# Optimization experiments

Measured on AMD Instinct MI355X. Metric: run time of the kernel, lower is better.

## Reference

```python
import jax, jax.numpy as jnp
import numpy as np

B, N, IN_F, E, H, A = 8, 1024, 1024, 256, 4, 64
ALPHA = 0.2          # leaky relu slope
NEG = -9e15          # mask value from original code


def setup_inputs() -> dict:
    key = jax.random.key(0)
    k = jax.random.split(key, 7)
    x = jax.random.normal(k[0], (B * N, IN_F), dtype=jnp.float32)
    adj = jax.random.randint(k[1], (B, N, N), 0, 2, dtype=jnp.int32)
    # per-head GAT params: W (H, IN_F, E); a split into a1, a2 (H, E) each,
    # since cat([Wh_i, Wh_j]) @ a == Wh_i @ a1 + Wh_j @ a2 exactly.
    W = jax.random.normal(k[2], (H, IN_F, E), dtype=jnp.float32) * 0.05
    a1 = jax.random.normal(k[3], (H, E), dtype=jnp.float32) * 0.05
    a2 = jax.random.normal(k[4], (H, E), dtype=jnp.float32) * 0.05
    W_act = jax.random.normal(k[5], (H * E, A), dtype=jnp.float32) * 0.05
    b_act = jnp.zeros((A,), dtype=jnp.float32)
    return {"x": x, "adj": adj, "W": W, "a1": a1, "a2": a2,
            "W_act": W_act, "b_act": b_act}


def reference(x, adj, W, a1, a2, W_act, b_act):
    b, n, _ = adj.shape
    xr = x.reshape(b, n, -1)                                   # (B, N, IN_F)
    Wh = jnp.einsum('bni,hio->hbno', xr, W)                    # (H, B, N, E)
    f1 = jnp.einsum('hbno,ho->hbn', Wh, a1)                    # a . Wh_i part
    f2 = jnp.einsum('hbno,ho->hbn', Wh, a2)                    # a . Wh_j part
    e = jax.nn.leaky_relu(f1[..., :, None] + f2[..., None, :], ALPHA)  # (H,B,N,N)
    e = jnp.where(adj[None] > 0, e, NEG)
    att = jax.nn.softmax(e, axis=-1)                           # masked softmax
    h_prime = jnp.einsum('hbnm,hbmo->hbno', att, Wh)           # (H, B, N, E)
    h_prime = jax.nn.elu(h_prime)                              # concat=True -> elu
    feat = jnp.transpose(h_prime, (1, 2, 0, 3)).reshape(b * n, H * E)
    return feat @ W_act + b_act                                # (B*N, A)
```

## Files before the change

kernel.cpp:

```cpp
#include <hip/hip_runtime.h>
#include <stdint.h>

typedef __attribute__((ext_vector_type(8))) short short8;
typedef __attribute__((ext_vector_type(4))) float f32x4;
typedef __attribute__((ext_vector_type(16))) float f32x16;


__device__ __forceinline__ float b2f(unsigned short u) {
    union { unsigned int i; float f; } v; v.i = ((unsigned int)u) << 16; return v.f;
}
__device__ __forceinline__ unsigned short f2b(float f) {
    union { float f; unsigned int i; } v; v.f = f;
    unsigned int u = v.i;
    u = (u + 0x7FFFu + ((u >> 16) & 1u)) >> 16;
    return (unsigned short)u;
}
__device__ __forceinline__ void glds16(const void* g, const void* l) {
    __builtin_amdgcn_global_load_lds(
        (const __attribute__((address_space(1))) unsigned int*)g,
        (__attribute__((address_space(3))) unsigned int*)l, 16, 0, 0);
}

__device__ __forceinline__ void cvt8(const void* in, unsigned short* out,
                                     int f, int grp) {
    if (f) {
        ((ushort4*)out)[grp * 2]     = ((const ushort4*)in)[grp * 2];
        ((ushort4*)out)[grp * 2 + 1] = ((const ushort4*)in)[grp * 2 + 1];
    } else {
        const float4* p = (const float4*)in + (size_t)grp * 2;
        float4 a = p[0], b = p[1];
        ushort4 o0, o1;
        o0.x = f2b(a.x); o0.y = f2b(a.y); o0.z = f2b(a.z); o0.w = f2b(a.w);
        o1.x = f2b(b.x); o1.y = f2b(b.y); o1.z = f2b(b.z); o1.w = f2b(b.w);
        ((ushort4*)out)[grp * 2]     = o0;
        ((ushort4*)out)[grp * 2 + 1] = o1;
    }
}

__global__ void prep_small(const unsigned int* __restrict__ x,
                           const void* __restrict__ a1, const void* __restrict__ a2,
                           const void* __restrict__ bact,
                           unsigned short* __restrict__ a1b,
                           unsigned short* __restrict__ a2b,
                           unsigned short* __restrict__ bactb,
                           int* __restrict__ flag) {
    __shared__ int sflag;
    int tid = threadIdx.x;
    if (tid < 64) {
        unsigned int wv = x[tid];
        unsigned int e = (wv >> 7) & 0xFF;
        unsigned long long m = __ballot(e >= 100 && e <= 140);
        if (tid == 0) { sflag = (__popcll(m) >= 48) ? 1 : 0; flag[0] = sflag; }
    }
    __syncthreads();
    int f = sflag;
    if (tid < 128) cvt8(a1, a1b, f, tid);
    else           cvt8(a2, a2b, f, tid - 128);
    if (tid < 8)   cvt8(bact, bactb, f, tid);
}

__global__ void conv8(const void* __restrict__ in, unsigned short* __restrict__ out,
                      const int* __restrict__ flag, int total8) {
    int i = blockIdx.x * 256 + threadIdx.x;
    if (i >= total8) return;
    cvt8(in, out, *flag, i);
}

__global__ __launch_bounds__(256) void t2_all(
        const void* __restrict__ Win, const void* __restrict__ Wactin,
        unsigned short* __restrict__ WT, unsigned short* __restrict__ WactT,
        const int* __restrict__ flag) {
    __shared__ unsigned int tile[64 * 65];
    int z = blockIdx.z;
    const void* in; unsigned short* out; int C, bt;
    if (z < 4) { in = Win; out = WT; C = 256; bt = z; }
    else { if (blockIdx.x != 0) return; in = Wactin; out = WactT; C = 64; bt = 0; }
    int t = threadIdx.x;
    int c0 = blockIdx.x * 64;
    int r0 = blockIdx.y * 64;
    int rl = t >> 2;
    int cc = (t & 3) * 16;
    size_t ibase = ((size_t)bt * 1024 + (r0 + rl)) * C + c0 + cc;
    unsigned short v[16];
    if (*flag) {
        const unsigned short* p = (const unsigned short*)in + ibase;
        short8 a = *(const short8*)p;
        short8 b = *(const short8*)(p + 8);
#pragma unroll
        for (int j = 0; j < 8; j++) { v[j] = (unsigned short)a[j]; v[8 + j] = (unsigned short)b[j]; }
    } else {
        const float* p = (const float*)in + ibase;
#pragma unroll
        for (int j = 0; j < 16; j++) v[j] = f2b(p[j]);
    }
#pragma unroll
    for (int j = 0; j < 16; j++)
        tile[(cc + j) * 65 + rl] = v[j];
    __syncthreads();
    int cl = t >> 2;
    int rch = (t & 3) * 16;
    unsigned short o[16];
#pragma unroll
    for (int j = 0; j < 16; j++)
        o[j] = (unsigned short)tile[cl * 65 + rch + j];
    unsigned short* op = out + ((size_t)bt * C + (c0 + cl)) * 1024 + r0 + rch;
#pragma unroll
    for (int q = 0; q < 4; q++) {
        ushort4 s; s.x = o[q*4]; s.y = o[q*4+1]; s.z = o[q*4+2]; s.w = o[q*4+3];
        ((ushort4*)op)[q] = s;
    }
}

__global__ void pack_adj(const int* __restrict__ adj,
                         unsigned int* __restrict__ maskT) {
    int gid = blockIdx.x * 256 + threadIdx.x;
    int lane = threadIdx.x & 63;
    unsigned long long m = __ballot(adj[gid] > 0);
    if (lane == 0) {
        int lin = gid >> 6;
        int mw = (lin & 15) * 2;
        int bn = lin >> 4;
        int b = bn >> 10, n = bn & 1023;
        maskT[(size_t)(b * 32 + mw) * 1024 + n]     = (unsigned int)m;
        maskT[(size_t)(b * 32 + mw + 1) * 1024 + n] = (unsigned int)(m >> 32);
    }
}

__global__ __launch_bounds__(256) void k1_gemm(
        const unsigned short* __restrict__ x,
        const unsigned short* __restrict__ WT,
        unsigned short* __restrict__ WhF) {
    __shared__ unsigned short smA[8 * 512];
    __shared__ unsigned short smB[8 * 512];
    int tid = threadIdx.x;
    int w = tid >> 6, lane = tid & 63;
    int lr = lane & 15, lq = lane >> 4;
    int col0 = blockIdx.x * 128;
    int row0 = blockIdx.y * 128;
    int h = col0 >> 8;
    int e_base = col0 & 255;
    int b = row0 >> 10;
    int m_base = row0 & 1023;
    int wr = w >> 1, wc = w & 1;

    f32x4 acc[4][4] = {};

    for (int k0 = 0; k0 < 1024; k0 += 32) {
        __syncthreads();
#pragma unroll
        for (int s = 0; s < 2; s++) {
            int g = 2 * w + s;
            const unsigned short* srcA =
                x + (size_t)(row0 + g * 16 + lr) * 1024 + k0 + lq * 8;
            glds16(srcA, &smA[g * 512]);
            const unsigned short* srcB =
                WT + (size_t)(h * 256 + e_base + g * 16 + lr) * 1024 + k0 + lq * 8;
            glds16(srcB, &smB[g * 512]);
        }
        __syncthreads();
        short8 af[4], bf[4];
#pragma unroll
        for (int i = 0; i < 4; i++)
            af[i] = *(const short8*)&smA[(wr * 4 + i) * 512 + lane * 8];
#pragma unroll
        for (int j = 0; j < 4; j++)
            bf[j] = *(const short8*)&smB[(wc * 4 + j) * 512 + lane * 8];
#pragma unroll
        for (int i = 0; i < 4; i++)
#pragma unroll
            for (int j = 0; j < 4; j++)
                acc[i][j] = __builtin_amdgcn_mfma_f32_16x16x32_bf16(
                    af[i], bf[j], acc[i][j], 0, 0, 0);
    }

    int hb = h * 8 + b;
#pragma unroll
    for (int i = 0; i < 4; i++) {
#pragma unroll
        for (int j = 0; j < 4; j++) {
            int e = e_base + (wc * 4 + j) * 16 + lr;
            int et = e >> 5, e31 = e & 31;
            int m16 = (m_base >> 4) + wr * 4 + i;
            ushort4 vs;
            vs.x = f2b(acc[i][j][0]);
            vs.y = f2b(acc[i][j][1]);
            vs.z = f2b(acc[i][j][2]);
            vs.w = f2b(acc[i][j][3]);
            size_t idx = ((size_t)((hb * 8 + et) * 64 + m16) * 512)
                         + ((lq >> 1) * 32 + e31) * 8 + (lq & 1) * 4;
            *(ushort4*)&WhF[idx] = vs;
        }
    }
}

__global__ void k1b_f12(const unsigned short* __restrict__ WhF,
                        const unsigned short* __restrict__ a1,
                        const unsigned short* __restrict__ a2,
                        float* __restrict__ f1, float* __restrict__ f2) {
    int hb = blockIdx.y;
    int n = blockIdx.x * 256 + threadIdx.x;
    int h = hb >> 3;
    int m16 = n >> 4, l5m = (n >> 3) & 1, m7 = n & 7;
    const unsigned short* base = WhF + (size_t)hb * 8 * 64 * 512
                                 + (size_t)(l5m * 32) * 8 + m7;
    float s1 = 0.f, s2 = 0.f;
    for (int e = 0; e < 256; e++) {
        int et = e >> 5, e31 = e & 31;
        float wv = b2f(base[(size_t)(et * 64 + m16) * 512 + e31 * 8]);
        s1 += wv * b2f(a1[h * 256 + e]);
        s2 += wv * b2f(a2[h * 256 + e]);
    }
    f1[hb * 1024 + n] = s1;
    f2[hb * 1024 + n] = s2;
}

__global__ __launch_bounds__(256, 2) void k2_attn(
        const unsigned short* __restrict__ WhF,
        const unsigned int* __restrict__ maskT,
        const float* __restrict__ f1, const float* __restrict__ f2,
        unsigned short* __restrict__ feat) {
    int tid = threadIdx.x;
    int w = tid >> 6, lane = tid & 63;
    int l5 = lane >> 5, l31 = lane & 31;
    int bid = blockIdx.x;
    int xcd = bid & 7, idx = bid >> 3;
    int hb = xcd + 8 * (idx >> 4);
    int sub = idx & 15;
    int wid = sub * 4 + w;
    int rg = wid >> 1;
    int ehalf = wid & 1;
    int n0 = rg * 32;
    int h = hb >> 3, b = hb & 7;
    int row = n0 + l31;
    float f1n = f1[hb * 1024 + row];
    const unsigned short* whb = WhF + (size_t)(hb * 8 + ehalf * 4) * 64 * 512
                                + lane * 8;
    const unsigned int* mrow = maskT + (size_t)b * 32 * 1024 + row;
    const float* f2row = f2 + hb * 1024;

    f32x16 acc[4] = {};
    float den = 0.f;

    short8 buf[2][4][2];
#pragma unroll
    for (int et = 0; et < 4; et++)
#pragma unroll
        for (int ks = 0; ks < 2; ks++)
            buf[0][et][ks] = *(const short8*)(whb + (size_t)(et * 64 + ks) * 512);

#pragma unroll 2
    for (int m0 = 0; m0 < 1024; m0 += 32) {
        int p = (m0 >> 5) & 1;
        if (m0 + 32 < 1024) {
            int m16n = (m0 >> 4) + 2;
#pragma unroll
            for (int et = 0; et < 4; et++)
#pragma unroll
                for (int ks = 0; ks < 2; ks++)
                    buf[p ^ 1][et][ks] =
                        *(const short8*)(whb + (size_t)(et * 64 + m16n + ks) * 512);
        }
        unsigned int mw = mrow[(size_t)(m0 >> 5) * 1024];
        float4 fA0 = *(const float4*)(f2row + m0 + l5 * 8);
        float4 fA1 = *(const float4*)(f2row + m0 + l5 * 8 + 4);
        float4 fB0 = *(const float4*)(f2row + m0 + 16 + l5 * 8);
        float4 fB1 = *(const float4*)(f2row + m0 + 16 + l5 * 8 + 4);
        float fm[16] = {fA0.x,fA0.y,fA0.z,fA0.w, fA1.x,fA1.y,fA1.z,fA1.w,
                        fB0.x,fB0.y,fB0.z,fB0.w, fB1.x,fB1.y,fB1.z,fB1.w};
        short8 af[2];
#pragma unroll
        for (int ks = 0; ks < 2; ks++) {
#pragma unroll
            for (int j = 0; j < 8; j++) {
                float t_ = f1n + fm[ks * 8 + j];
                float e_ = fmaxf(t_, 0.2f * t_);
                float pv = ((mw >> (ks * 16 + l5 * 8 + j)) & 1u) ? __expf(e_) : 0.f;
                unsigned short pb = f2b(pv);
                af[ks][j] = (short)pb;
                den += b2f(pb);
            }
        }
#pragma unroll
        for (int et = 0; et < 4; et++)
#pragma unroll
            for (int ks = 0; ks < 2; ks++)
                acc[et] = __builtin_amdgcn_mfma_f32_32x32x16_bf16(
                    af[ks], buf[p][et][ks], acc[et], 0, 0, 0);
    }

    den += __shfl_xor(den, 32, 64);

#pragma unroll
    for (int reg = 0; reg < 16; reg++) {
        int r = (reg & 3) + 8 * (reg >> 2) + 4 * l5;
        float dr = __shfl(den, r, 64);
        float rdr = 1.0f / dr;
        int nn = n0 + r;
#pragma unroll
        for (int et = 0; et < 4; et++) {
            int e = ehalf * 128 + et * 32 + l31;
            float v = acc[et][reg] * rdr;
            float o = v > 0.f ? v : __expf(v) - 1.f;
            feat[(size_t)(b * 1024 + nn) * 1024 + h * 256 + e] = f2b(o);
        }
    }
}

__global__ __launch_bounds__(256) void k3_out(
        const unsigned short* __restrict__ feat,
        const unsigned short* __restrict__ WactT,
        const unsigned short* __restrict__ bact,
        void* __restrict__ out, const int* __restrict__ flag) {
    __shared__ unsigned short smA[2 * 512];
    __shared__ unsigned short smB[4 * 512];
    int tid = threadIdx.x;
    int w = tid >> 6, lane = tid & 63;
    int lr = lane & 15, lq = lane >> 4;
    int row0 = blockIdx.x * 32;
    int g = w & 1, ch = w >> 1;
    int bf16out = *flag;
    f32x4 acc[2] = {};

    for (int k0 = 0; k0 < 1024; k0 += 32) {
        __syncthreads();
        if (w < 2) {
            const unsigned short* src =
                feat + (size_t)(row0 + w * 16 + lr) * 1024 + k0 + lq * 8;
            glds16(src, &smA[w * 512]);
        } else {
#pragma unroll
            for (int s = 0; s < 2; s++) {
                int t = (w - 2) * 2 + s;
                const unsigned short* src =
                    WactT + (size_t)(t * 16 + lr) * 1024 + k0 + lq * 8;
                glds16(src, &smB[t * 512]);
            }
        }
        __syncthreads();
        short8 af = *(const short8*)&smA[g * 512 + lane * 8];
#pragma unroll
        for (int j = 0; j < 2; j++) {
            short8 bf = *(const short8*)&smB[(ch * 2 + j) * 512 + lane * 8];
            acc[j] = __builtin_amdgcn_mfma_f32_16x16x32_bf16(af, bf, acc[j], 0, 0, 0);
        }
    }
#pragma unroll
    for (int j = 0; j < 2; j++) {
        int col = ch * 32 + j * 16 + lr;
        float bv = b2f(bact[col]);
#pragma unroll
        for (int rr = 0; rr < 4; rr++) {
            int r = row0 + g * 16 + lq * 4 + rr;
            float val = acc[j][rr] + bv;
            if (bf16out) ((unsigned short*)out)[(size_t)r * 64 + col] = f2b(val);
            else         ((float*)out)[(size_t)r * 64 + col] = val;
        }
    }
}

extern "C" void kernel_launch(void* const* d_in, const int* in_sizes, int n_in,
                              void* d_out, int out_size, void* d_ws, size_t ws_size,
                              hipStream_t stream) {
    const void* x    = d_in[0];
    const int*  adj  = (const int*)d_in[1];
    const void* W    = d_in[2];
    const void* a1   = d_in[3];
    const void* a2   = d_in[4];
    const void* Wact = d_in[5];
    const void* bact = d_in[6];

    char* ws = (char*)d_ws;
    unsigned short* WhF   = (unsigned short*)(ws);
    unsigned short* xb    = (unsigned short*)(ws + 16777216);
    unsigned short* feat  = (unsigned short*)(ws + 16777216);
    unsigned short* WT    = (unsigned short*)(ws + 33554432);
    unsigned int*   maskT = (unsigned int*)(ws + 33554432);
    unsigned short* WactT = (unsigned short*)(ws + 35651584);
    float*          f1    = (float*)(ws + 35782656);
    float*          f2    = (float*)(ws + 35913728);
    unsigned short* a1b   = (unsigned short*)(ws + 36044800);
    unsigned short* a2b   = (unsigned short*)(ws + 36046848);
    unsigned short* bactb = (unsigned short*)(ws + 36048896);
    int*            flag  = (int*)(ws + 36049024);
    if (ws_size < (size_t)36049040) return;

    prep_small<<<1, 256, 0, stream>>>((const unsigned int*)x, a1, a2, bact,
                                      a1b, a2b, bactb, flag);
    conv8<<<4096, 256, 0, stream>>>(x, xb, flag, 1048576);
    t2_all<<<dim3(4, 16, 5), 256, 0, stream>>>(W, Wact, WT, WactT, flag);
    k1_gemm<<<dim3(8, 64), 256, 0, stream>>>(xb, WT, WhF);
    pack_adj<<<32768, 256, 0, stream>>>(adj, maskT);
    k1b_f12<<<dim3(4, 32), 256, 0, stream>>>(WhF, a1b, a2b, f1, f2);
    k2_attn<<<512, 256, 0, stream>>>(WhF, maskT, f1, f2, feat);
    k3_out<<<256, 256, 0, stream>>>(feat, WactT, bactb, d_out, flag);
}
```

Baseline: 239.8 us.

## Split attention key range across wave pairs and vectorise f1/f2 with atomics

The attention kernel changes from splitting the embedding dimension across waves to splitting the key range in halves. Each wave now computes all 256 output columns for half the keys, so the softmax weights are computed once per row instead of twice. Partial accumulators and denominators are combined through shared memory, which costs extra LDS traffic, higher register pressure from 8 accumulators, and the loss of the explicit double-buffered prefetch. The f1/f2 kernel now uses vectorised short8 loads split over embedding chunks and combines them with atomic adds, which needs a new zeroing kernel. It also pre-scales f1/f2 by log2(e) so exp2f can replace __expf, and the bf16 conversion becomes truncation instead of round-to-nearest.

```diff
diff --git a/kernel.cpp b/kernel.cpp
--- a/kernel.cpp
+++ b/kernel.cpp
@@ -64,6 +64,10 @@
     int i = blockIdx.x * 256 + threadIdx.x;
     if (i >= total8) return;
     cvt8(in, out, *flag, i);
+}
+
+__global__ void zero_kern(float4* __restrict__ p) {
+    p[blockIdx.x * 256 + threadIdx.x] = float4{0.f, 0.f, 0.f, 0.f};
 }
 
 __global__ __launch_bounds__(256) void t2_all(
@@ -198,20 +202,31 @@
                         const unsigned short* __restrict__ a2,
                         float* __restrict__ f1, float* __restrict__ f2) {
     int hb = blockIdx.y;
-    int n = blockIdx.x * 256 + threadIdx.x;
+    int ec = blockIdx.x;
+    int t = threadIdx.x;
     int h = hb >> 3;
-    int m16 = n >> 4, l5m = (n >> 3) & 1, m7 = n & 7;
     const unsigned short* base = WhF + (size_t)hb * 8 * 64 * 512
-                                 + (size_t)(l5m * 32) * 8 + m7;
-    float s1 = 0.f, s2 = 0.f;
-    for (int e = 0; e < 256; e++) {
+        + (size_t)(t >> 1) * 512 + ((t & 1) * 32) * 8;
+    float s1[8] = {}, s2[8] = {};
+    for (int ee = 0; ee < 64; ee++) {
+        int e = ec * 64 + ee;
         int et = e >> 5, e31 = e & 31;
-        float wv = b2f(base[(size_t)(et * 64 + m16) * 512 + e31 * 8]);
-        s1 += wv * b2f(a1[h * 256 + e]);
-        s2 += wv * b2f(a2[h * 256 + e]);
-    }
-    f1[hb * 1024 + n] = s1;
-    f2[hb * 1024 + n] = s2;
+        float a1e = b2f(a1[h * 256 + e]);
+        float a2e = b2f(a2[h * 256 + e]);
+        short8 v = *(const short8*)(base + (size_t)(et * 64) * 512 + e31 * 8);
+#pragma unroll
+        for (int j = 0; j < 8; j++) {
+            float wv = b2f((unsigned short)v[j]);
+            s1[j] += wv * a1e;
+            s2[j] += wv * a2e;
+        }
+    }
+    const float LOG2E = 1.44269504f;
+#pragma unroll
+    for (int j = 0; j < 8; j++) {
+        atomicAdd(&f1[hb * 1024 + t * 8 + j], s1[j] * LOG2E);
+        atomicAdd(&f2[hb * 1024 + t * 8 + j], s2[j] * LOG2E);
+    }
 }
 
 __global__ __launch_bounds__(256, 2) void k2_attn(
@@ -219,89 +234,102 @@
         const unsigned int* __restrict__ maskT,
         const float* __restrict__ f1, const float* __restrict__ f2,
         unsigned short* __restrict__ feat) {
+    __shared__ float cmb[4][64][65];
+    __shared__ float dend[4][32];
     int tid = threadIdx.x;
     int w = tid >> 6, lane = tid & 63;
     int l5 = lane >> 5, l31 = lane & 31;
     int bid = blockIdx.x;
     int xcd = bid & 7, idx = bid >> 3;
     int hb = xcd + 8 * (idx >> 4);
-    int sub = idx & 15;
-    int wid = sub * 4 + w;
-    int rg = wid >> 1;
-    int ehalf = wid & 1;
+    int pair = idx & 15;
+    int rg = pair * 2 + (w & 1);
+    int mh = w >> 1;
     int n0 = rg * 32;
     int h = hb >> 3, b = hb & 7;
     int row = n0 + l31;
     float f1n = f1[hb * 1024 + row];
-    const unsigned short* whb = WhF + (size_t)(hb * 8 + ehalf * 4) * 64 * 512
-                                + lane * 8;
+    const unsigned short* whb = WhF + (size_t)hb * 8 * 64 * 512 + lane * 8;
     const unsigned int* mrow = maskT + (size_t)b * 32 * 1024 + row;
     const float* f2row = f2 + hb * 1024;
 
-    f32x16 acc[4] = {};
+    f32x16 acc[8] = {};
     float den = 0.f;
 
-    short8 buf[2][4][2];
-#pragma unroll
-    for (int et = 0; et < 4; et++)
-#pragma unroll
-        for (int ks = 0; ks < 2; ks++)
-            buf[0][et][ks] = *(const short8*)(whb + (size_t)(et * 64 + ks) * 512);
-
-#pragma unroll 2
-    for (int m0 = 0; m0 < 1024; m0 += 32) {
-        int p = (m0 >> 5) & 1;
-        if (m0 + 32 < 1024) {
-            int m16n = (m0 >> 4) + 2;
-#pragma unroll
-            for (int et = 0; et < 4; et++)
-#pragma unroll
-                for (int ks = 0; ks < 2; ks++)
-                    buf[p ^ 1][et][ks] =
-                        *(const short8*)(whb + (size_t)(et * 64 + m16n + ks) * 512);
-        }
-        unsigned int mw = mrow[(size_t)(m0 >> 5) * 1024];
+    int m_lo = mh * 512, m_hi = m_lo + 512;
+    for (int m0 = m_lo; m0 < m_hi; m0 += 32) {
+        int m16 = m0 >> 4;
+        short8 fr[8][2];
+#pragma unroll
+        for (int et = 0; et < 8; et++)
+#pragma unroll
+            for (int ks = 0; ks < 2; ks++)
+                fr[et][ks] = *(const short8*)(whb + (size_t)(et * 64 + m16 + ks) * 512);
+
+        unsigned int mws = mrow[(size_t)(m0 >> 5) * 1024] >> (l5 * 8);
         float4 fA0 = *(const float4*)(f2row + m0 + l5 * 8);
         float4 fA1 = *(const float4*)(f2row + m0 + l5 * 8 + 4);
         float4 fB0 = *(const float4*)(f2row + m0 + 16 + l5 * 8);
         float4 fB1 = *(const float4*)(f2row + m0 + 16 + l5 * 8 + 4);
         float fm[16] = {fA0.x,fA0.y,fA0.z,fA0.w, fA1.x,fA1.y,fA1.z,fA1.w,
                         fB0.x,fB0.y,fB0.z,fB0.w, fB1.x,fB1.y,fB1.z,fB1.w};
-        short8 af[2];
+        union { unsigned int u[4]; short8 v; } af[2];
 #pragma unroll
         for (int ks = 0; ks < 2; ks++) {
 #pragma unroll
-            for (int j = 0; j < 8; j++) {
-                float t_ = f1n + fm[ks * 8 + j];
-                float e_ = fmaxf(t_, 0.2f * t_);
-                float pv = ((mw >> (ks * 16 + l5 * 8 + j)) & 1u) ? __expf(e_) : 0.f;
-                unsigned short pb = f2b(pv);
-                af[ks][j] = (short)pb;
-                den += b2f(pb);
+            for (int pr = 0; pr < 4; pr++) {
+                unsigned int ub[2];
+#pragma unroll
+                for (int q = 0; q < 2; q++) {
+                    int j = pr * 2 + q;
+                    float tL = f1n + fm[ks * 8 + j];
+                    float eL = fmaxf(tL, 0.2f * tL);
+                    float pv = ((mws >> (ks * 16 + j)) & 1u) ? exp2f(eL) : 0.f;
+                    union { float f; unsigned int i; } pu; pu.f = pv;
+                    ub[q] = pu.i & 0xFFFF0000u;
+                    union { unsigned int i; float f; } tb; tb.i = ub[q];
+                    den += tb.f;
+                }
+                af[ks].u[pr] = (ub[0] >> 16) | ub[1];
             }
         }
 #pragma unroll
-        for (int et = 0; et < 4; et++)
+        for (int et = 0; et < 8; et++)
 #pragma unroll
             for (int ks = 0; ks < 2; ks++)
                 acc[et] = __builtin_amdgcn_mfma_f32_32x32x16_bf16(
-                    af[ks], buf[p][et][ks], acc[et], 0, 0, 0);
+                    af[ks].v, fr[et][ks], acc[et], 0, 0, 0);
     }
 
     den += __shfl_xor(den, 32, 64);
 
+    int give = (mh == 0) ? 4 : 0;
+    int keep = (mh == 0) ? 0 : 4;
+#pragma unroll
+    for (int t = 0; t < 4; t++)
+#pragma unroll
+        for (int reg = 0; reg < 16; reg++)
+            cmb[w][lane][t * 16 + reg] = acc[give + t][reg];
+    if (lane < 32) dend[w][l31] = den;
+    __syncthreads();
+    int pw = w ^ 2;
+    float den_tot = den + dend[pw][l31];
+    float rdr_all[16];
 #pragma unroll
     for (int reg = 0; reg < 16; reg++) {
         int r = (reg & 3) + 8 * (reg >> 2) + 4 * l5;
-        float dr = __shfl(den, r, 64);
-        float rdr = 1.0f / dr;
-        int nn = n0 + r;
-#pragma unroll
-        for (int et = 0; et < 4; et++) {
-            int e = ehalf * 128 + et * 32 + l31;
-            float v = acc[et][reg] * rdr;
+        rdr_all[reg] = 1.0f / __shfl(den_tot, r, 64);
+    }
+#pragma unroll
+    for (int t = 0; t < 4; t++) {
+        int et = keep + t;
+        int e = et * 32 + l31;
+#pragma unroll
+        for (int reg = 0; reg < 16; reg++) {
+            int r = (reg & 3) + 8 * (reg >> 2) + 4 * l5;
+            float v = (acc[et][reg] + cmb[pw][lane][t * 16 + reg]) * rdr_all[reg];
             float o = v > 0.f ? v : __expf(v) - 1.f;
-            feat[(size_t)(b * 1024 + nn) * 1024 + h * 256 + e] = f2b(o);
+            feat[(size_t)(b * 1024 + n0 + r) * 1024 + h * 256 + e] = f2b(o);
         }
     }
 }
@@ -388,9 +416,10 @@
                                       a1b, a2b, bactb, flag);
     conv8<<<4096, 256, 0, stream>>>(x, xb, flag, 1048576);
     t2_all<<<dim3(4, 16, 5), 256, 0, stream>>>(W, Wact, WT, WactT, flag);
+    zero_kern<<<64, 256, 0, stream>>>((float4*)f1);
     k1_gemm<<<dim3(8, 64), 256, 0, stream>>>(xb, WT, WhF);
     pack_adj<<<32768, 256, 0, stream>>>(adj, maskT);
-    k1b_f12<<<dim3(4, 32), 256, 0, stream>>>(WhF, a1b, a2b, f1, f2);
+    k1b_f12<<<dim3(4, 32), 128, 0, stream>>>(WhF, a1b, a2b, f1, f2);
     k2_attn<<<512, 256, 0, stream>>>(WhF, maskT, f1, f2, feat);
     k3_out<<<256, 256, 0, stream>>>(feat, WactT, bactb, d_out, flag);
 }
```

New measurement: 249.3 us. 1.04x slower.

## Fuse preprocessing kernels and fold f1/f2 projection into GEMM epilogue

Applied to the files above, without the earlier changes.

Merges the flag detection, x conversion, W/W_act transposes and small-parameter conversion into one launch, which also zeroes the f1/f2 buffers. The f1/f2 attention projections move out of a separate serial-loop kernel and into the k1_gemm epilogue: the fp32 accumulators are reduced with wave shuffles and added into f1/f2 with atomics. The projections are pre-scaled by log2(e) so the attention kernel can call exp2f instead of __expf. This removes two launches and a strided re-read of Wh, at the cost of atomic traffic and per-block recomputation of the input-format flag.

```diff
diff --git a/kernel.cpp b/kernel.cpp
--- a/kernel.cpp
+++ b/kernel.cpp
@@ -37,52 +37,62 @@
     }
 }
 
-__global__ void prep_small(const unsigned int* __restrict__ x,
-                           const void* __restrict__ a1, const void* __restrict__ a2,
-                           const void* __restrict__ bact,
-                           unsigned short* __restrict__ a1b,
-                           unsigned short* __restrict__ a2b,
-                           unsigned short* __restrict__ bactb,
-                           int* __restrict__ flag) {
+__global__ __launch_bounds__(256) void prep_all(
+        const unsigned int* __restrict__ x4,
+        const void* __restrict__ x, const void* __restrict__ W,
+        const void* __restrict__ Wact,
+        const void* __restrict__ a1, const void* __restrict__ a2,
+        const void* __restrict__ bact,
+        unsigned short* __restrict__ xb, unsigned short* __restrict__ WT,
+        unsigned short* __restrict__ WactT,
+        unsigned short* __restrict__ a1b, unsigned short* __restrict__ a2b,
+        unsigned short* __restrict__ bactb,
+        int* __restrict__ flag, float4* __restrict__ fz) {
+    __shared__ unsigned int tile[64 * 65];
     __shared__ int sflag;
     int tid = threadIdx.x;
+    int bid = blockIdx.x;
+    if (bid >= 4352 && bid < 4416) {
+        fz[(bid - 4352) * 256 + tid] = float4{0.f, 0.f, 0.f, 0.f};
+        return;
+    }
     if (tid < 64) {
-        unsigned int wv = x[tid];
+        unsigned int wv = x4[tid];
         unsigned int e = (wv >> 7) & 0xFF;
         unsigned long long m = __ballot(e >= 100 && e <= 140);
-        if (tid == 0) { sflag = (__popcll(m) >= 48) ? 1 : 0; flag[0] = sflag; }
+        if (tid == 0) sflag = (__popcll(m) >= 48) ? 1 : 0;
     }
     __syncthreads();
     int f = sflag;
-    if (tid < 128) cvt8(a1, a1b, f, tid);
-    else           cvt8(a2, a2b, f, tid - 128);
-    if (tid < 8)   cvt8(bact, bactb, f, tid);
-}
-
-__global__ void conv8(const void* __restrict__ in, unsigned short* __restrict__ out,
-                      const int* __restrict__ flag, int total8) {
-    int i = blockIdx.x * 256 + threadIdx.x;
-    if (i >= total8) return;
-    cvt8(in, out, *flag, i);
-}
-
-__global__ __launch_bounds__(256) void t2_all(
-        const void* __restrict__ Win, const void* __restrict__ Wactin,
-        unsigned short* __restrict__ WT, unsigned short* __restrict__ WactT,
-        const int* __restrict__ flag) {
-    __shared__ unsigned int tile[64 * 65];
-    int z = blockIdx.z;
-    const void* in; unsigned short* out; int C, bt;
-    if (z < 4) { in = Win; out = WT; C = 256; bt = z; }
-    else { if (blockIdx.x != 0) return; in = Wactin; out = WactT; C = 64; bt = 0; }
-    int t = threadIdx.x;
-    int c0 = blockIdx.x * 64;
-    int r0 = blockIdx.y * 64;
-    int rl = t >> 2;
-    int cc = (t & 3) * 16;
+
+    if (bid < 4096) {
+        cvt8(x, xb, f, bid * 256 + tid);
+        return;
+    }
+    if (bid == 4416) {
+        if (tid == 0) flag[0] = f;
+        if (tid < 128) cvt8(a1, a1b, f, tid);
+        else           cvt8(a2, a2b, f, tid - 128);
+        if (tid < 8)   cvt8(bact, bactb, f, tid);
+        return;
+    }
+    const void* in; unsigned short* out; int C, bt, c0, r0;
+    if (bid < 4352) {
+        int lb = bid - 4096;
+        in = W; out = WT; C = 256;
+        c0 = (lb & 3) * 64;
+        r0 = ((lb >> 2) & 15) * 64;
+        bt = lb >> 6;
+    } else {
+        int lb = bid - 4417;
+        in = Wact; out = WactT; C = 64;
+        c0 = 0; r0 = lb * 64; bt = 0;
+    }
+    int rl = tid >> 2;
+    int cc = (tid & 3) * 16;
     size_t ibase = ((size_t)bt * 1024 + (r0 + rl)) * C + c0 + cc;
     unsigned short v[16];
-    if (*flag) {
+    if (f) {
         const unsigned short* p = (const unsigned short*)in + ibase;
         short8 a = *(const short8*)p;
         short8 b = *(const short8*)(p + 8);
@@ -97,8 +107,8 @@
     for (int j = 0; j < 16; j++)
         tile[(cc + j) * 65 + rl] = v[j];
     __syncthreads();
-    int cl = t >> 2;
-    int rch = (t & 3) * 16;
+    int cl = tid >> 2;
+    int rch = (tid & 3) * 16;
     unsigned short o[16];
 #pragma unroll
     for (int j = 0; j < 16; j++)
@@ -129,7 +139,10 @@
 __global__ __launch_bounds__(256) void k1_gemm(
         const unsigned short* __restrict__ x,
         const unsigned short* __restrict__ WT,
-        unsigned short* __restrict__ WhF) {
+        unsigned short* __restrict__ WhF,
+        const unsigned short* __restrict__ a1b,
+        const unsigned short* __restrict__ a2b,
+        float* __restrict__ f1, float* __restrict__ f2) {
     __shared__ unsigned short smA[8 * 512];
     __shared__ unsigned short smB[8 * 512];
     int tid = threadIdx.x;
@@ -191,27 +204,36 @@
             *(ushort4*)&WhF[idx] = vs;
         }
     }
-}
-
-__global__ void k1b_f12(const unsigned short* __restrict__ WhF,
-                        const unsigned short* __restrict__ a1,
-                        const unsigned short* __restrict__ a2,
-                        float* __restrict__ f1, float* __restrict__ f2) {
-    int hb = blockIdx.y;
-    int n = blockIdx.x * 256 + threadIdx.x;
-    int h = hb >> 3;
-    int m16 = n >> 4, l5m = (n >> 3) & 1, m7 = n & 7;
-    const unsigned short* base = WhF + (size_t)hb * 8 * 64 * 512
-                                 + (size_t)(l5m * 32) * 8 + m7;
-    float s1 = 0.f, s2 = 0.f;
-    for (int e = 0; e < 256; e++) {
-        int et = e >> 5, e31 = e & 31;
-        float wv = b2f(base[(size_t)(et * 64 + m16) * 512 + e31 * 8]);
-        s1 += wv * b2f(a1[h * 256 + e]);
-        s2 += wv * b2f(a2[h * 256 + e]);
-    }
-    f1[hb * 1024 + n] = s1;
-    f2[hb * 1024 + n] = s2;
+
+    const float LOG2E = 1.44269504f;
+    float a1v[4], a2v[4];
+#pragma unroll
+    for (int j = 0; j < 4; j++) {
+        int e = e_base + (wc * 4 + j) * 16 + lr;
+        a1v[j] = b2f(a1b[h * 256 + e]);
+        a2v[j] = b2f(a2b[h * 256 + e]);
+    }
+#pragma unroll
+    for (int i = 0; i < 4; i++) {
+#pragma unroll
+        for (int reg = 0; reg < 4; reg++) {
+            float s1 = 0.f, s2 = 0.f;
+#pragma unroll
+            for (int j = 0; j < 4; j++) {
+                s1 += acc[i][j][reg] * a1v[j];
+                s2 += acc[i][j][reg] * a2v[j];
+            }
+            s1 += __shfl_xor(s1, 1, 64); s2 += __shfl_xor(s2, 1, 64);
+            s1 += __shfl_xor(s1, 2, 64); s2 += __shfl_xor(s2, 2, 64);
+            s1 += __shfl_xor(s1, 4, 64); s2 += __shfl_xor(s2, 4, 64);
+            s1 += __shfl_xor(s1, 8, 64); s2 += __shfl_xor(s2, 8, 64);
+            if (lr == 0) {
+                int m = m_base + (wr * 4 + i) * 16 + lq * 4 + reg;
+                atomicAdd(&f1[hb * 1024 + m], s1 * LOG2E);
+                atomicAdd(&f2[hb * 1024 + m], s2 * LOG2E);
+            }
+        }
+    }
 }
 
 __global__ __launch_bounds__(256, 2) void k2_attn(
@@ -274,7 +296,7 @@
             for (int j = 0; j < 8; j++) {
                 float t_ = f1n + fm[ks * 8 + j];
                 float e_ = fmaxf(t_, 0.2f * t_);
-                float pv = ((mw >> (ks * 16 + l5 * 8 + j)) & 1u) ? __expf(e_) : 0.f;
+                float pv = ((mw >> (ks * 16 + l5 * 8 + j)) & 1u) ? exp2f(e_) : 0.f;
                 unsigned short pb = f2b(pv);
                 af[ks][j] = (short)pb;
                 den += b2f(pb);
@@ -384,13 +406,11 @@
     int*            flag  = (int*)(ws + 36049024);
     if (ws_size < (size_t)36049040) return;
 
-    prep_small<<<1, 256, 0, stream>>>((const unsigned int*)x, a1, a2, bact,
-                                      a1b, a2b, bactb, flag);
-    conv8<<<4096, 256, 0, stream>>>(x, xb, flag, 1048576);
-    t2_all<<<dim3(4, 16, 5), 256, 0, stream>>>(W, Wact, WT, WactT, flag);
-    k1_gemm<<<dim3(8, 64), 256, 0, stream>>>(xb, WT, WhF);
+    prep_all<<<4433, 256, 0, stream>>>((const unsigned int*)x, x, W, Wact,
+                                       a1, a2, bact, xb, WT, WactT,
+                                       a1b, a2b, bactb, flag, (float4*)f1);
+    k1_gemm<<<dim3(8, 64), 256, 0, stream>>>(xb, WT, WhF, a1b, a2b, f1, f2);
     pack_adj<<<32768, 256, 0, stream>>>(adj, maskT);
-    k1b_f12<<<dim3(4, 32), 256, 0, stream>>>(WhF, a1b, a2b, f1, f2);
     k2_attn<<<512, 256, 0, stream>>>(WhF, maskT, f1, f2, feat);
     k3_out<<<256, 256, 0, stream>>>(feat, WactT, bactb, d_out, flag);
 }
```

Measured after the change: 222.1 us. -7.4%, faster.
